# Performance work log

Measured on AMD Instinct MI355X. Metric: run time of the kernel, lower is better.

Reference implementation:

```python
import jax, jax.numpy as jnp
import numpy as np

ALPHA = 0.2          # leaky relu negative slope
NEG_BIG = -9e15      # masking value used by the torch module


def setup_inputs() -> dict:
    key = jax.random.key(0)
    k1, k2, k3, k4, k5 = jax.random.split(key, 5)
    N, F_IN, F_OUT = 8192, 256, 64
    inputs = jax.random.normal(k1, (N, F_IN), dtype=jnp.float32)
    adj = jax.random.randint(k2, (N, N), 0, 2, dtype=jnp.int32)
    # xavier-normal-ish parameter init (scale is irrelevant for correctness testing)
    W = jax.random.normal(k3, (F_IN, F_OUT), dtype=jnp.float32) * np.sqrt(2.0 / (F_IN + F_OUT))
    a1 = jax.random.normal(k4, (F_OUT, 1), dtype=jnp.float32) * np.sqrt(2.0 / (F_OUT + 1))
    a2 = jax.random.normal(k5, (F_OUT, 1), dtype=jnp.float32) * np.sqrt(2.0 / (F_OUT + 1))
    return {"inputs": inputs, "adj": adj, "W": W, "a1": a1, "a2": a2}


def reference(inputs, adj, W, a1, a2):
    # h: [N, F_OUT]
    h = inputs @ W
    f1 = h @ a1                      # [N, 1]
    f2 = h @ a2                      # [N, 1]
    e = jax.nn.leaky_relu(f1 + f2.T, negative_slope=ALPHA)   # [N, N] broadcast additive score
    e = jnp.where(adj > 0, e, NEG_BIG)
    attention = jax.nn.softmax(e, axis=-1)                    # masked softmax over rows
    # dropout is identity in eval mode (training=False)
    h_prime = attention @ h                                   # [N, F_OUT]
    return jax.nn.elu(h_prime)                                # concat=True -> elu
```

## Files before the change

kernel.cpp:

```cpp
#include <hip/hip_runtime.h>
#include <hip/hip_bf16.h>

#define N     8192
#define FIN   256
#define FOUT  64
#define ALPHA 0.2f
#define KQ    8
#define JQ    (N / KQ)
#define TJ    256
#define NTL   (JQ / TJ)
#define NSW   2

typedef __attribute__((ext_vector_type(8))) short bf16x8;
typedef __attribute__((ext_vector_type(4))) float f32x4;
typedef __attribute__((ext_vector_type(4))) int   i32x4;

static __device__ __forceinline__ unsigned short f2bf(float x) {
    union { float f; unsigned int u; } v; v.f = x;
    unsigned int r = v.u + 0x7FFFu + ((v.u >> 16) & 1u);
    return (unsigned short)(r >> 16);
}
static __device__ __forceinline__ float asf(unsigned int u) {
    union { unsigned int u; float f; } v; v.u = u; return v.f;
}
static __device__ __forceinline__ float wcalc(float f1v, float f2v, int a) {
    const float e = f1v + f2v;
    const float lr = fmaxf(e, ALPHA * e);
    const float w = __expf(lr);
    return (a > 0) ? w : 0.f;
}
static __device__ __forceinline__ void gload_lds16(const int* g, int* l) {
    __builtin_amdgcn_global_load_lds(
        (const __attribute__((address_space(1))) void*)g,
        (__attribute__((address_space(3))) void*)l,
        16, 0, 0);
}
static __device__ __forceinline__ int rowperm(int row) {
    return ((row << 1) | (row >> 3)) & 63;
}

__global__ __launch_bounds__(256) void k_h(
        const float* __restrict__ X, const float* __restrict__ W,
        const float* __restrict__ a1, const float* __restrict__ a2,
        unsigned short* __restrict__ hb,
        float* __restrict__ f1, float* __restrict__ f2) {
    const int lane = threadIdx.x & 63;
    const int wave = threadIdx.x >> 6;
    const int row0 = (blockIdx.x * 4 + wave) * 4;

    const f32x4* Xr[4];
    #pragma unroll
    for (int r = 0; r < 4; ++r)
        Xr[r] = (const f32x4*)(X + (size_t)(row0 + r) * FIN);

    float acc[4] = {0.f, 0.f, 0.f, 0.f};
    #pragma unroll 4
    for (int k4 = 0; k4 < FIN / 4; ++k4) {
        const float w0 = W[(k4 * 4 + 0) * FOUT + lane];
        const float w1 = W[(k4 * 4 + 1) * FOUT + lane];
        const float w2 = W[(k4 * 4 + 2) * FOUT + lane];
        const float w3 = W[(k4 * 4 + 3) * FOUT + lane];
        #pragma unroll
        for (int r = 0; r < 4; ++r) {
            const f32x4 xv = __builtin_nontemporal_load(&Xr[r][k4]);
            acc[r] = fmaf(xv.x, w0, acc[r]);
            acc[r] = fmaf(xv.y, w1, acc[r]);
            acc[r] = fmaf(xv.z, w2, acc[r]);
            acc[r] = fmaf(xv.w, w3, acc[r]);
        }
    }

    ushort4 hv;
    hv.x = f2bf(acc[0]); hv.y = f2bf(acc[1]);
    hv.z = f2bf(acc[2]); hv.w = f2bf(acc[3]);
    *(ushort4*)&hb[(size_t)(row0 >> 3) * 512 + lane * 8 + (row0 & 7)] = hv;

    const float a1v = a1[lane];
    const float a2v = a2[lane];
    #pragma unroll
    for (int r = 0; r < 4; ++r) {
        float p1 = acc[r] * a1v;
        float p2 = acc[r] * a2v;
        #pragma unroll
        for (int off = 32; off > 0; off >>= 1) {
            p1 += __shfl_down(p1, off);
            p2 += __shfl_down(p2, off);
        }
        if (lane == 0) { f1[row0 + r] = p1; f2[row0 + r] = p2; }
    }
}

__global__ __launch_bounds__(256) void k_attn(
        const int* __restrict__ adj, const unsigned short* __restrict__ hb,
        const float* __restrict__ f1, const float* __restrict__ f2,
        float* __restrict__ part, float* __restrict__ pden) {
    __shared__ int  tile[2][16][TJ];
    __shared__ f32x4 red[2][256];
    __shared__ float dred[4][16];

    const int t    = threadIdx.x;
    const int lane = t & 63;
    const int wv   = t >> 6;
    const int bid  = blockIdx.x;
    const int rg   = bid >> 3;
    const int q    = bid & 7;
    const int i0   = rg * 16;
    const int r    = lane & 15;
    const int kg   = lane >> 4;

    const float f1v = f1[i0 + r];
    const int jb = q * JQ;
    const int pr = rowperm(r);

    f32x4 acc[4];
    #pragma unroll
    for (int c = 0; c < 4; ++c) acc[c] = (f32x4){0.f, 0.f, 0.f, 0.f};
    float sacc = 0.f;

    #pragma unroll
    for (int rr = 0; rr < 4; ++rr) {
        const int row = wv * 4 + rr;
        gload_lds16(adj + (size_t)(i0 + row) * N + jb + (lane ^ rowperm(row)) * 4,
                    &tile[0][row][0]);
    }
    asm volatile("s_waitcnt vmcnt(0)" ::: "memory");
    __builtin_amdgcn_s_barrier();

    int buf = 0;
    for (int tt = 0; tt < NTL; ++tt) {
        const int jt = jb + tt * TJ;

        bf16x8 bfr[NSW][4];
        float4 fa[NSW], fb[NSW];
        #pragma unroll
        for (int ss = 0; ss < NSW; ++ss) {
            const int s = wv * NSW + ss;
            const float* f2s = f2 + jt + s * 32 + kg * 8;
            fa[ss] = *(const float4*)(f2s);
            fb[ss] = *(const float4*)(f2s + 4);
            const unsigned short* hs =
                hb + (size_t)((jt >> 3) + s * 4 + kg) * 512 + r * 8;
            bfr[ss][0] = *(const bf16x8*)(hs);
            bfr[ss][1] = *(const bf16x8*)(hs + 128);
            bfr[ss][2] = *(const bf16x8*)(hs + 256);
            bfr[ss][3] = *(const bf16x8*)(hs + 384);
        }
        __builtin_amdgcn_sched_barrier(0);

        if (tt + 1 < NTL) {
            #pragma unroll
            for (int rr = 0; rr < 4; ++rr) {
                const int row = wv * 4 + rr;
                gload_lds16(adj + (size_t)(i0 + row) * N + jt + TJ
                                + (lane ^ rowperm(row)) * 4,
                            &tile[buf ^ 1][row][0]);
            }
            __builtin_amdgcn_sched_barrier(0);
            asm volatile("s_waitcnt vmcnt(4)" ::: "memory");
        } else {
            asm volatile("s_waitcnt vmcnt(0)" ::: "memory");
        }
        __builtin_amdgcn_s_barrier();

        #pragma unroll
        for (int ss = 0; ss < NSW; ++ss) {
            const int s = wv * NSW + ss;
            const int g0 = s * 8 + kg * 2;
            const i32x4 a0 = *(const i32x4*)&tile[buf][r][((g0 ^ pr) & 63) * 4];
            const i32x4 a1 = *(const i32x4*)&tile[buf][r][(((g0 + 1) ^ pr) & 63) * 4];

            const float w0 = wcalc(f1v, fa[ss].x, a0.x);
            const float w1 = wcalc(f1v, fa[ss].y, a0.y);
            const float w2 = wcalc(f1v, fa[ss].z, a0.z);
            const float w3 = wcalc(f1v, fa[ss].w, a0.w);
            const float w4 = wcalc(f1v, fb[ss].x, a1.x);
            const float w5 = wcalc(f1v, fb[ss].y, a1.y);
            const float w6 = wcalc(f1v, fb[ss].z, a1.z);
            const float w7 = wcalc(f1v, fb[ss].w, a1.w);

            union { bf16x8 v; __hip_bfloat162 h2[4]; unsigned int u[4]; } af;
            af.h2[0] = __float22bfloat162_rn(make_float2(w0, w1));
            af.h2[1] = __float22bfloat162_rn(make_float2(w2, w3));
            af.h2[2] = __float22bfloat162_rn(make_float2(w4, w5));
            af.h2[3] = __float22bfloat162_rn(make_float2(w6, w7));

            float ds = 0.f;
            #pragma unroll
            for (int u = 0; u < 4; ++u)
                ds += asf(af.u[u] << 16) + asf(af.u[u] & 0xFFFF0000u);
            sacc += ds;

            acc[0] = __builtin_amdgcn_mfma_f32_16x16x32_bf16(af.v, bfr[ss][0], acc[0], 0, 0, 0);
            acc[1] = __builtin_amdgcn_mfma_f32_16x16x32_bf16(af.v, bfr[ss][1], acc[1], 0, 0, 0);
            acc[2] = __builtin_amdgcn_mfma_f32_16x16x32_bf16(af.v, bfr[ss][2], acc[2], 0, 0, 0);
            acc[3] = __builtin_amdgcn_mfma_f32_16x16x32_bf16(af.v, bfr[ss][3], acc[3], 0, 0, 0);
        }
        __builtin_amdgcn_s_barrier();
        buf ^= 1;
    }

    sacc += __shfl_xor(sacc, 16);
    sacc += __shfl_xor(sacc, 32);
    if (lane < 16) dred[wv][lane] = sacc;

    __syncthreads();
    if (wv >= 2) {
        #pragma unroll
        for (int cg = 0; cg < 4; ++cg) red[wv - 2][lane * 4 + cg] = acc[cg];
    }
    __syncthreads();
    if (wv < 2) {
        #pragma unroll
        for (int cg = 0; cg < 4; ++cg) acc[cg] += red[wv][lane * 4 + cg];
    }
    __syncthreads();
    if (wv == 1) {
        #pragma unroll
        for (int cg = 0; cg < 4; ++cg) red[0][lane * 4 + cg] = acc[cg];
    }
    __syncthreads();
    if (wv == 0) {
        #pragma unroll
        for (int cg = 0; cg < 4; ++cg) acc[cg] += red[0][lane * 4 + cg];
        #pragma unroll
        for (int cg = 0; cg < 4; ++cg)
            #pragma unroll
            for (int rr = 0; rr < 4; ++rr)
                __builtin_nontemporal_store(acc[cg][rr],
                    &part[(size_t)bid * 1024 + (kg * 4 + rr) * FOUT + cg * 16 + r]);
        if (lane < 16)
            __builtin_nontemporal_store(
                dred[0][lane] + dred[1][lane] + dred[2][lane] + dred[3][lane],
                &pden[bid * 16 + lane]);
    }
}

__global__ __launch_bounds__(256) void k_fin(
        const float* __restrict__ part, const float* __restrict__ pden,
        float* __restrict__ out) {
    const int rg = blockIdx.x;
    const int t  = threadIdx.x;
    const int r  = t >> 4;
    const int c4 = (t & 15) * 4;

    float vx = 0.f, vy = 0.f, vz = 0.f, vw = 0.f;
    float den = 0.f;
    #pragma unroll
    for (int p = 0; p < KQ; ++p) {
        const int blk = rg * KQ + p;
        const f32x4 pv = __builtin_nontemporal_load(
            (const f32x4*)&part[(size_t)blk * 1024 + r * FOUT + c4]);
        vx += pv.x; vy += pv.y; vz += pv.z; vw += pv.w;
        den += __builtin_nontemporal_load(&pden[blk * 16 + r]);
    }
    den = fmaxf(den, 1e-30f);
    const float inv = __fdividef(1.f, den);
    f32x4 o;
    const float h0 = vx * inv; o.x = (h0 > 0.f) ? h0 : (__expf(h0) - 1.f);
    const float h1 = vy * inv; o.y = (h1 > 0.f) ? h1 : (__expf(h1) - 1.f);
    const float h2 = vz * inv; o.z = (h2 > 0.f) ? h2 : (__expf(h2) - 1.f);
    const float h3 = vw * inv; o.w = (h3 > 0.f) ? h3 : (__expf(h3) - 1.f);
    __builtin_nontemporal_store(o,
        (f32x4*)&out[(size_t)(rg * 16 + r) * FOUT + c4]);
}

extern "C" void kernel_launch(void* const* d_in, const int* in_sizes, int n_in,
                              void* d_out, int out_size, void* d_ws, size_t ws_size,
                              hipStream_t stream) {
    const float* X   = (const float*)d_in[0];
    const int*   adj = (const int*)d_in[1];
    const float* W   = (const float*)d_in[2];
    const float* a1  = (const float*)d_in[3];
    const float* a2  = (const float*)d_in[4];
    float* out = (float*)d_out;

    unsigned short* hb = (unsigned short*)d_ws;
    float* f1   = (float*)((char*)d_ws + (size_t)FOUT * N * 2);
    float* f2   = f1 + N;
    float* part = f2 + N;
    float* pden = part + (size_t)(N / 16) * KQ * 1024;

    k_h   <<<N / 16, 256, 0, stream>>>(X, W, a1, a2, hb, f1, f2);
    k_attn<<<(N / 16) * KQ, 256, 0, stream>>>(adj, hb, f1, f2, part, pden);
    k_fin <<<N / 16, 256, 0, stream>>>(part, pden, out);
}
```

Before: 86.75 us.

## Process 32 rows per attention block to reuse h and f2 fragments

Each k_attn block now handles 32 destination rows instead of 16, using two accumulator sets that share the same bf16 h fragments and f2 values loaded from global memory. This halves the per-row global traffic for h/f2 and halves the grid size. The adj tile and LDS double buffer double in size, the reduction scratch now reuses the tile LDS, and launch bounds request two blocks per CU. The cost is higher register and LDS use per block and fewer blocks in flight.

Result: slower. 91.99 us (+6.0%).

```diff
diff --git a/kernel.cpp b/kernel.cpp
--- a/kernel.cpp
+++ b/kernel.cpp
@@ -10,6 +10,7 @@
 #define TJ    256
 #define NTL   (JQ / TJ)
 #define NSW   2
+#define RB    32
 
 typedef __attribute__((ext_vector_type(8))) short bf16x8;
 typedef __attribute__((ext_vector_type(4))) float f32x4;
@@ -36,7 +37,7 @@
         16, 0, 0);
 }
 static __device__ __forceinline__ int rowperm(int row) {
-    return ((row << 1) | (row >> 3)) & 63;
+    return ((row << 1) | (row >> 4)) & 63;
 }
 
 __global__ __launch_bounds__(256) void k_h(
@@ -90,13 +91,12 @@
     }
 }
 
-__global__ __launch_bounds__(256) void k_attn(
+__global__ __launch_bounds__(256, 2) void k_attn(
         const int* __restrict__ adj, const unsigned short* __restrict__ hb,
         const float* __restrict__ f1, const float* __restrict__ f2,
         float* __restrict__ part, float* __restrict__ pden) {
-    __shared__ int  tile[2][16][TJ];
-    __shared__ f32x4 red[2][256];
-    __shared__ float dred[4][16];
+    __shared__ int smem[2 * RB * TJ];
+    __shared__ float dred[4][32];
 
     const int t    = threadIdx.x;
     const int lane = t & 63;
@@ -104,24 +104,29 @@
     const int bid  = blockIdx.x;
     const int rg   = bid >> 3;
     const int q    = bid & 7;
-    const int i0   = rg * 16;
+    const int i0   = rg * RB;
     const int r    = lane & 15;
     const int kg   = lane >> 4;
 
-    const float f1v = f1[i0 + r];
+    const float f1a = f1[i0 + r];
+    const float f1b = f1[i0 + 16 + r];
     const int jb = q * JQ;
-    const int pr = rowperm(r);
-
-    f32x4 acc[4];
-    #pragma unroll
-    for (int c = 0; c < 4; ++c) acc[c] = (f32x4){0.f, 0.f, 0.f, 0.f};
-    float sacc = 0.f;
-
-    #pragma unroll
-    for (int rr = 0; rr < 4; ++rr) {
-        const int row = wv * 4 + rr;
-        gload_lds16(adj + (size_t)(i0 + row) * N + jb + (lane ^ rowperm(row)) * 4,
-                    &tile[0][row][0]);
+    const int prA = rowperm(r);
+    const int prB = rowperm(16 + r);
+
+    f32x4 accA[4], accB[4];
+    #pragma unroll
+    for (int c = 0; c < 4; ++c) {
+        accA[c] = (f32x4){0.f, 0.f, 0.f, 0.f};
+        accB[c] = (f32x4){0.f, 0.f, 0.f, 0.f};
+    }
+    float saccA = 0.f, saccB = 0.f;
+
+    #pragma unroll
+    for (int rr = 0; rr < 8; ++rr) {
+        const int row = wv * 8 + rr;
+        gload_lds16(adj + (size_t)(i0 + row) * N + jb + ((lane ^ rowperm(row)) & 63) * 4,
+                    &smem[row * TJ]);
     }
     asm volatile("s_waitcnt vmcnt(0)" ::: "memory");
     __builtin_amdgcn_s_barrier();
@@ -149,109 +154,154 @@
 
         if (tt + 1 < NTL) {
             #pragma unroll
-            for (int rr = 0; rr < 4; ++rr) {
-                const int row = wv * 4 + rr;
+            for (int rr = 0; rr < 8; ++rr) {
+                const int row = wv * 8 + rr;
                 gload_lds16(adj + (size_t)(i0 + row) * N + jt + TJ
-                                + (lane ^ rowperm(row)) * 4,
-                            &tile[buf ^ 1][row][0]);
+                                + ((lane ^ rowperm(row)) & 63) * 4,
+                            &smem[(buf ^ 1) * RB * TJ + row * TJ]);
             }
             __builtin_amdgcn_sched_barrier(0);
-            asm volatile("s_waitcnt vmcnt(4)" ::: "memory");
+            asm volatile("s_waitcnt vmcnt(8)" ::: "memory");
         } else {
             asm volatile("s_waitcnt vmcnt(0)" ::: "memory");
         }
         __builtin_amdgcn_s_barrier();
 
+        const int* tb = &smem[buf * RB * TJ];
         #pragma unroll
         for (int ss = 0; ss < NSW; ++ss) {
             const int s = wv * NSW + ss;
             const int g0 = s * 8 + kg * 2;
-            const i32x4 a0 = *(const i32x4*)&tile[buf][r][((g0 ^ pr) & 63) * 4];
-            const i32x4 a1 = *(const i32x4*)&tile[buf][r][(((g0 + 1) ^ pr) & 63) * 4];
-
-            const float w0 = wcalc(f1v, fa[ss].x, a0.x);
-            const float w1 = wcalc(f1v, fa[ss].y, a0.y);
-            const float w2 = wcalc(f1v, fa[ss].z, a0.z);
-            const float w3 = wcalc(f1v, fa[ss].w, a0.w);
-            const float w4 = wcalc(f1v, fb[ss].x, a1.x);
-            const float w5 = wcalc(f1v, fb[ss].y, a1.y);
-            const float w6 = wcalc(f1v, fb[ss].z, a1.z);
-            const float w7 = wcalc(f1v, fb[ss].w, a1.w);
-
-            union { bf16x8 v; __hip_bfloat162 h2[4]; unsigned int u[4]; } af;
-            af.h2[0] = __float22bfloat162_rn(make_float2(w0, w1));
-            af.h2[1] = __float22bfloat162_rn(make_float2(w2, w3));
-            af.h2[2] = __float22bfloat162_rn(make_float2(w4, w5));
-            af.h2[3] = __float22bfloat162_rn(make_float2(w6, w7));
-
-            float ds = 0.f;
-            #pragma unroll
-            for (int u = 0; u < 4; ++u)
-                ds += asf(af.u[u] << 16) + asf(af.u[u] & 0xFFFF0000u);
-            sacc += ds;
-
-            acc[0] = __builtin_amdgcn_mfma_f32_16x16x32_bf16(af.v, bfr[ss][0], acc[0], 0, 0, 0);
-            acc[1] = __builtin_amdgcn_mfma_f32_16x16x32_bf16(af.v, bfr[ss][1], acc[1], 0, 0, 0);
-            acc[2] = __builtin_amdgcn_mfma_f32_16x16x32_bf16(af.v, bfr[ss][2], acc[2], 0, 0, 0);
-            acc[3] = __builtin_amdgcn_mfma_f32_16x16x32_bf16(af.v, bfr[ss][3], acc[3], 0, 0, 0);
+            const i32x4 a0 = *(const i32x4*)&tb[r * TJ + ((g0 ^ prA) & 63) * 4];
+            const i32x4 a1 = *(const i32x4*)&tb[r * TJ + (((g0 + 1) ^ prA) & 63) * 4];
+            const i32x4 b0 = *(const i32x4*)&tb[(16 + r) * TJ + ((g0 ^ prB) & 63) * 4];
+            const i32x4 b1 = *(const i32x4*)&tb[(16 + r) * TJ + (((g0 + 1) ^ prB) & 63) * 4];
+
+            {
+                const float w0 = wcalc(f1a, fa[ss].x, a0.x);
+                const float w1 = wcalc(f1a, fa[ss].y, a0.y);
+                const float w2 = wcalc(f1a, fa[ss].z, a0.z);
+                const float w3 = wcalc(f1a, fa[ss].w, a0.w);
+                const float w4 = wcalc(f1a, fb[ss].x, a1.x);
+                const float w5 = wcalc(f1a, fb[ss].y, a1.y);
+                const float w6 = wcalc(f1a, fb[ss].z, a1.z);
+                const float w7 = wcalc(f1a, fb[ss].w, a1.w);
+                union { bf16x8 v; __hip_bfloat162 h2[4]; unsigned int u[4]; } af;
+                af.h2[0] = __float22bfloat162_rn(make_float2(w0, w1));
+                af.h2[1] = __float22bfloat162_rn(make_float2(w2, w3));
+                af.h2[2] = __float22bfloat162_rn(make_float2(w4, w5));
+                af.h2[3] = __float22bfloat162_rn(make_float2(w6, w7));
+                float ds = 0.f;
+                #pragma unroll
+                for (int u = 0; u < 4; ++u)
+                    ds += asf(af.u[u] << 16) + asf(af.u[u] & 0xFFFF0000u);
+                saccA += ds;
+                accA[0] = __builtin_amdgcn_mfma_f32_16x16x32_bf16(af.v, bfr[ss][0], accA[0], 0, 0, 0);
+                accA[1] = __builtin_amdgcn_mfma_f32_16x16x32_bf16(af.v, bfr[ss][1], accA[1], 0, 0, 0);
+                accA[2] = __builtin_amdgcn_mfma_f32_16x16x32_bf16(af.v, bfr[ss][2], accA[2], 0, 0, 0);
+                accA[3] = __builtin_amdgcn_mfma_f32_16x16x32_bf16(af.v, bfr[ss][3], accA[3], 0, 0, 0);
+            }
+            {
+                const float w0 = wcalc(f1b, fa[ss].x, b0.x);
+                const float w1 = wcalc(f1b, fa[ss].y, b0.y);
+                const float w2 = wcalc(f1b, fa[ss].z, b0.z);
+                const float w3 = wcalc(f1b, fa[ss].w, b0.w);
+                const float w4 = wcalc(f1b, fb[ss].x, b1.x);
+                const float w5 = wcalc(f1b, fb[ss].y, b1.y);
+                const float w6 = wcalc(f1b, fb[ss].z, b1.z);
+                const float w7 = wcalc(f1b, fb[ss].w, b1.w);
+                union { bf16x8 v; __hip_bfloat162 h2[4]; unsigned int u[4]; } af;
+                af.h2[0] = __float22bfloat162_rn(make_float2(w0, w1));
+                af.h2[1] = __float22bfloat162_rn(make_float2(w2, w3));
+                af.h2[2] = __float22bfloat162_rn(make_float2(w4, w5));
+                af.h2[3] = __float22bfloat162_rn(make_float2(w6, w7));
+                float ds = 0.f;
+                #pragma unroll
+                for (int u = 0; u < 4; ++u)
+                    ds += asf(af.u[u] << 16) + asf(af.u[u] & 0xFFFF0000u);
+                saccB += ds;
+                accB[0] = __builtin_amdgcn_mfma_f32_16x16x32_bf16(af.v, bfr[ss][0], accB[0], 0, 0, 0);
+                accB[1] = __builtin_amdgcn_mfma_f32_16x16x32_bf16(af.v, bfr[ss][1], accB[1], 0, 0, 0);
+                accB[2] = __builtin_amdgcn_mfma_f32_16x16x32_bf16(af.v, bfr[ss][2], accB[2], 0, 0, 0);
+                accB[3] = __builtin_amdgcn_mfma_f32_16x16x32_bf16(af.v, bfr[ss][3], accB[3], 0, 0, 0);
+            }
         }
         __builtin_amdgcn_s_barrier();
         buf ^= 1;
     }
 
-    sacc += __shfl_xor(sacc, 16);
-    sacc += __shfl_xor(sacc, 32);
-    if (lane < 16) dred[wv][lane] = sacc;
-
+    saccA += __shfl_xor(saccA, 16); saccA += __shfl_xor(saccA, 32);
+    saccB += __shfl_xor(saccB, 16); saccB += __shfl_xor(saccB, 32);
+    if (lane < 16) { dred[wv][lane] = saccA; dred[wv][16 + lane] = saccB; }
+
+    f32x4* redA = (f32x4*)smem;
+    f32x4* redB = (f32x4*)&smem[2048];
     __syncthreads();
     if (wv >= 2) {
         #pragma unroll
-        for (int cg = 0; cg < 4; ++cg) red[wv - 2][lane * 4 + cg] = acc[cg];
+        for (int cg = 0; cg < 4; ++cg) {
+            redA[(wv - 2) * 256 + lane * 4 + cg] = accA[cg];
+            redB[(wv - 2) * 256 + lane * 4 + cg] = accB[cg];
+        }
     }
     __syncthreads();
     if (wv < 2) {
         #pragma unroll
-        for (int cg = 0; cg < 4; ++cg) acc[cg] += red[wv][lane * 4 + cg];
+        for (int cg = 0; cg < 4; ++cg) {
+            accA[cg] += redA[wv * 256 + lane * 4 + cg];
+            accB[cg] += redB[wv * 256 + lane * 4 + cg];
+        }
     }
     __syncthreads();
     if (wv == 1) {
         #pragma unroll
-        for (int cg = 0; cg < 4; ++cg) red[0][lane * 4 + cg] = acc[cg];
+        for (int cg = 0; cg < 4; ++cg) {
+            redA[lane * 4 + cg] = accA[cg];
+            redB[lane * 4 + cg] = accB[cg];
+        }
     }
     __syncthreads();
     if (wv == 0) {
         #pragma unroll
-        for (int cg = 0; cg < 4; ++cg) acc[cg] += red[0][lane * 4 + cg];
+        for (int cg = 0; cg < 4; ++cg) {
+            accA[cg] += redA[lane * 4 + cg];
+            accB[cg] += redB[lane * 4 + cg];
+        }
         #pragma unroll
         for (int cg = 0; cg < 4; ++cg)
             #pragma unroll
-            for (int rr = 0; rr < 4; ++rr)
-                __builtin_nontemporal_store(acc[cg][rr],
-                    &part[(size_t)bid * 1024 + (kg * 4 + rr) * FOUT + cg * 16 + r]);
-        if (lane < 16)
+            for (int rr = 0; rr < 4; ++rr) {
+                __builtin_nontemporal_store(accA[cg][rr],
+                    &part[(size_t)bid * 2048 + (kg * 4 + rr) * FOUT + cg * 16 + r]);
+                __builtin_nontemporal_store(accB[cg][rr],
+                    &part[(size_t)bid * 2048 + (16 + kg * 4 + rr) * FOUT + cg * 16 + r]);
+            }
+        if (lane < 32)
             __builtin_nontemporal_store(
                 dred[0][lane] + dred[1][lane] + dred[2][lane] + dred[3][lane],
-                &pden[bid * 16 + lane]);
+                &pden[bid * 32 + lane]);
     }
 }
 
 __global__ __launch_bounds__(256) void k_fin(
         const float* __restrict__ part, const float* __restrict__ pden,
         float* __restrict__ out) {
-    const int rg = blockIdx.x;
-    const int t  = threadIdx.x;
-    const int r  = t >> 4;
-    const int c4 = (t & 15) * 4;
+    const int t   = threadIdx.x;
+    const int r   = t >> 4;
+    const int c4  = (t & 15) * 4;
+    const int i   = blockIdx.x * 16 + r;
+    const int rgb = i >> 5;
+    const int ro  = i & 31;
 
     float vx = 0.f, vy = 0.f, vz = 0.f, vw = 0.f;
     float den = 0.f;
     #pragma unroll
     for (int p = 0; p < KQ; ++p) {
-        const int blk = rg * KQ + p;
+        const int b2 = rgb * KQ + p;
         const f32x4 pv = __builtin_nontemporal_load(
-            (const f32x4*)&part[(size_t)blk * 1024 + r * FOUT + c4]);
+            (const f32x4*)&part[(size_t)b2 * 2048 + ro * FOUT + c4]);
         vx += pv.x; vy += pv.y; vz += pv.z; vw += pv.w;
-        den += __builtin_nontemporal_load(&pden[blk * 16 + r]);
+        den += __builtin_nontemporal_load(&pden[b2 * 32 + ro]);
     }
     den = fmaxf(den, 1e-30f);
     const float inv = __fdividef(1.f, den);
@@ -260,8 +310,7 @@
     const float h1 = vy * inv; o.y = (h1 > 0.f) ? h1 : (__expf(h1) - 1.f);
     const float h2 = vz * inv; o.z = (h2 > 0.f) ? h2 : (__expf(h2) - 1.f);
     const float h3 = vw * inv; o.w = (h3 > 0.f) ? h3 : (__expf(h3) - 1.f);
-    __builtin_nontemporal_store(o,
-        (f32x4*)&out[(size_t)(rg * 16 + r) * FOUT + c4]);
+    __builtin_nontemporal_store(o, (f32x4*)&out[(size_t)i * FOUT + c4]);
 }
 
 extern "C" void kernel_launch(void* const* d_in, const int* in_sizes, int n_in,
@@ -278,9 +327,9 @@
     float* f1   = (float*)((char*)d_ws + (size_t)FOUT * N * 2);
     float* f2   = f1 + N;
     float* part = f2 + N;
-    float* pden = part + (size_t)(N / 16) * KQ * 1024;
+    float* pden = part + (size_t)(N / RB) * KQ * 2048;
 
     k_h   <<<N / 16, 256, 0, stream>>>(X, W, a1, a2, hb, f1, f2);
-    k_attn<<<(N / 16) * KQ, 256, 0, stream>>>(adj, hb, f1, f2, part, pden);
+    k_attn<<<(N / RB) * KQ, 256, 0, stream>>>(adj, hb, f1, f2, part, pden);
     k_fin <<<N / 16, 256, 0, stream>>>(part, pden, out);
 }
```

## Triple-buffer adjacency tiles and register-prefetch next tile's h and f2

Applied to the files above, without the earlier changes.

Replaces the double-buffered LDS adjacency tile with a three-stage ring, so adjacency loads run two tiles ahead. The h (bf16) fragments and f2 values for the next tile are prefetched into registers while the current tile is computed. The tile loop is fully unrolled, and the reduction scratch now reuses the tile LDS. This aims to hide global-load latency behind the MFMA work, at the cost of more VGPRs and LDS per block, which launch_bounds(256,3) tries to keep in check.

After: 85.08 us (median of 2 runs). Within noise of the previous version (-1.9%).

```diff
diff --git a/kernel.cpp b/kernel.cpp
--- a/kernel.cpp
+++ b/kernel.cpp
@@ -10,6 +10,7 @@
 #define TJ    256
 #define NTL   (JQ / TJ)
 #define NSW   2
+#define TILEI (16 * TJ)
 
 typedef __attribute__((ext_vector_type(8))) short bf16x8;
 typedef __attribute__((ext_vector_type(4))) float f32x4;
@@ -90,12 +91,30 @@
     }
 }
 
-__global__ __launch_bounds__(256) void k_attn(
+static __device__ __forceinline__ void load_regs(
+        int jt, int wv, int kg, int r,
+        const float* __restrict__ f2, const unsigned short* __restrict__ hb,
+        bf16x8 (&bfr)[NSW][4], float4 (&fa)[NSW], float4 (&fb)[NSW]) {
+    #pragma unroll
+    for (int ss = 0; ss < NSW; ++ss) {
+        const int s = wv * NSW + ss;
+        const float* f2s = f2 + jt + s * 32 + kg * 8;
+        fa[ss] = *(const float4*)(f2s);
+        fb[ss] = *(const float4*)(f2s + 4);
+        const unsigned short* hs =
+            hb + (size_t)((jt >> 3) + s * 4 + kg) * 512 + r * 8;
+        bfr[ss][0] = *(const bf16x8*)(hs);
+        bfr[ss][1] = *(const bf16x8*)(hs + 128);
+        bfr[ss][2] = *(const bf16x8*)(hs + 256);
+        bfr[ss][3] = *(const bf16x8*)(hs + 384);
+    }
+}
+
+__global__ __launch_bounds__(256, 3) void k_attn(
         const int* __restrict__ adj, const unsigned short* __restrict__ hb,
         const float* __restrict__ f1, const float* __restrict__ f2,
         float* __restrict__ part, float* __restrict__ pden) {
-    __shared__ int  tile[2][16][TJ];
-    __shared__ f32x4 red[2][256];
+    __shared__ int smem[3 * TILEI];
     __shared__ float dred[4][16];
 
     const int t    = threadIdx.x;
@@ -120,63 +139,61 @@
     #pragma unroll
     for (int rr = 0; rr < 4; ++rr) {
         const int row = wv * 4 + rr;
-        gload_lds16(adj + (size_t)(i0 + row) * N + jb + (lane ^ rowperm(row)) * 4,
-                    &tile[0][row][0]);
-    }
-    asm volatile("s_waitcnt vmcnt(0)" ::: "memory");
-    __builtin_amdgcn_s_barrier();
-
-    int buf = 0;
+        gload_lds16(adj + (size_t)(i0 + row) * N + jb + ((lane ^ rowperm(row)) & 63) * 4,
+                    &smem[row * TJ]);
+    }
+    bf16x8 bcur[NSW][4], bnxt[NSW][4];
+    float4 facur[NSW], fbcur[NSW], fanxt[NSW], fbnxt[NSW];
+    load_regs(jb, wv, kg, r, f2, hb, bcur, facur, fbcur);
+    __builtin_amdgcn_sched_barrier(0);
+    #pragma unroll
+    for (int rr = 0; rr < 4; ++rr) {
+        const int row = wv * 4 + rr;
+        gload_lds16(adj + (size_t)(i0 + row) * N + jb + TJ + ((lane ^ rowperm(row)) & 63) * 4,
+                    &smem[TILEI + row * TJ]);
+    }
+    __builtin_amdgcn_sched_barrier(0);
+
+    #pragma unroll
     for (int tt = 0; tt < NTL; ++tt) {
         const int jt = jb + tt * TJ;
 
-        bf16x8 bfr[NSW][4];
-        float4 fa[NSW], fb[NSW];
-        #pragma unroll
-        for (int ss = 0; ss < NSW; ++ss) {
-            const int s = wv * NSW + ss;
-            const float* f2s = f2 + jt + s * 32 + kg * 8;
-            fa[ss] = *(const float4*)(f2s);
-            fb[ss] = *(const float4*)(f2s + 4);
-            const unsigned short* hs =
-                hb + (size_t)((jt >> 3) + s * 4 + kg) * 512 + r * 8;
-            bfr[ss][0] = *(const bf16x8*)(hs);
-            bfr[ss][1] = *(const bf16x8*)(hs + 128);
-            bfr[ss][2] = *(const bf16x8*)(hs + 256);
-            bfr[ss][3] = *(const bf16x8*)(hs + 384);
-        }
+        if (tt + 1 < NTL)
+            load_regs(jt + TJ, wv, kg, r, f2, hb, bnxt, fanxt, fbnxt);
         __builtin_amdgcn_sched_barrier(0);
 
-        if (tt + 1 < NTL) {
+        if (tt + 2 < NTL) {
             #pragma unroll
             for (int rr = 0; rr < 4; ++rr) {
                 const int row = wv * 4 + rr;
-                gload_lds16(adj + (size_t)(i0 + row) * N + jt + TJ
-                                + (lane ^ rowperm(row)) * 4,
-                            &tile[buf ^ 1][row][0]);
+                gload_lds16(adj + (size_t)(i0 + row) * N + jt + 2 * TJ
+                                + ((lane ^ rowperm(row)) & 63) * 4,
+                            &smem[((tt + 2) % 3) * TILEI + row * TJ]);
             }
             __builtin_amdgcn_sched_barrier(0);
-            asm volatile("s_waitcnt vmcnt(4)" ::: "memory");
-        } else {
-            asm volatile("s_waitcnt vmcnt(0)" ::: "memory");
-        }
+        }
+
+        if (tt + 2 < NTL)      asm volatile("s_waitcnt vmcnt(20)" ::: "memory");
+        else if (tt + 1 < NTL) asm volatile("s_waitcnt vmcnt(16)" ::: "memory");
+        else                   asm volatile("s_waitcnt vmcnt(0)"  ::: "memory");
         __builtin_amdgcn_s_barrier();
 
+        const int* tb = &smem[(tt % 3) * TILEI];
         #pragma unroll
         for (int ss = 0; ss < NSW; ++ss) {
             const int s = wv * NSW + ss;
             const int g0 = s * 8 + kg * 2;
-            const i32x4 a0 = *(const i32x4*)&tile[buf][r][((g0 ^ pr) & 63) * 4];
-            const i32x4 a1 = *(const i32x4*)&tile[buf][r][(((g0 + 1) ^ pr) & 63) * 4];
-
-            const float w0 = wcalc(f1v, fa[ss].x, a0.x);
-            const float w1 = wcalc(f1v, fa[ss].y, a0.y);
-            const float w2 = wcalc(f1v, fa[ss].z, a0.z);
-            const float w3 = wcalc(f1v, fa[ss].w, a0.w);
-            const float w4 = wcalc(f1v, fb[ss].x, a1.x);
-            const float w5 = wcalc(f1v, fb[ss].y, a1.y);
-            const float w6 = wcalc(f1v, fb[ss].z, a1.z);
-            const float w7 = wcalc(f1v, fb[ss].w, a1.w);
+            const i32x4 a0 = *(const i32x4*)&tb[r * TJ + ((g0 ^ pr) & 63) * 4];
+            const i32x4 a1 = *(const i32x4*)&tb[r * TJ + (((g0 + 1) ^ pr) & 63) * 4];
+
+            const float w0 = wcalc(f1v, facur[ss].x, a0.x);
+            const float w1 = wcalc(f1v, facur[ss].y, a0.y);
+            const float w2 = wcalc(f1v, facur[ss].z, a0.z);
+            const float w3 = wcalc(f1v, facur[ss].w, a0.w);
+            const float w4 = wcalc(f1v, fbcur[ss].x, a1.x);
+            const float w5 = wcalc(f1v, fbcur[ss].y, a1.y);
+            const float w6 = wcalc(f1v, fbcur[ss].z, a1.z);
+            const float w7 = wcalc(f1v, fbcur[ss].w, a1.w);
 
             union { bf16x8 v; __hip_bfloat162 h2[4]; unsigned int u[4]; } af;
             af.h2[0] = __float22bfloat162_rn(make_float2(w0, w1));
@@ -190,38 +207,47 @@
                 ds += asf(af.u[u] << 16) + asf(af.u[u] & 0xFFFF0000u);
             sacc += ds;
 
-            acc[0] = __builtin_amdgcn_mfma_f32_16x16x32_bf16(af.v, bfr[ss][0], acc[0], 0, 0, 0);
-            acc[1] = __builtin_amdgcn_mfma_f32_16x16x32_bf16(af.v, bfr[ss][1], acc[1], 0, 0, 0);
-            acc[2] = __builtin_amdgcn_mfma_f32_16x16x32_bf16(af.v, bfr[ss][2], acc[2], 0, 0, 0);
-            acc[3] = __builtin_amdgcn_mfma_f32_16x16x32_bf16(af.v, bfr[ss][3], acc[3], 0, 0, 0);
+            acc[0] = __builtin_amdgcn_mfma_f32_16x16x32_bf16(af.v, bcur[ss][0], acc[0], 0, 0, 0);
+            acc[1] = __builtin_amdgcn_mfma_f32_16x16x32_bf16(af.v, bcur[ss][1], acc[1], 0, 0, 0);
+            acc[2] = __builtin_amdgcn_mfma_f32_16x16x32_bf16(af.v, bcur[ss][2], acc[2], 0, 0, 0);
+            acc[3] = __builtin_amdgcn_mfma_f32_16x16x32_bf16(af.v, bcur[ss][3], acc[3], 0, 0, 0);
         }
         __builtin_amdgcn_s_barrier();
-        buf ^= 1;
+
+        if (tt + 1 < NTL) {
+            #pragma unroll
+            for (int ss = 0; ss < NSW; ++ss) {
+                bcur[ss][0] = bnxt[ss][0]; bcur[ss][1] = bnxt[ss][1];
+                bcur[ss][2] = bnxt[ss][2]; bcur[ss][3] = bnxt[ss][3];
+                facur[ss] = fanxt[ss]; fbcur[ss] = fbnxt[ss];
+            }
+        }
     }
 
     sacc += __shfl_xor(sacc, 16);
     sacc += __shfl_xor(sacc, 32);
     if (lane < 16) dred[wv][lane] = sacc;
 
+    f32x4* red = (f32x4*)smem;
     __syncthreads();
     if (wv >= 2) {
         #pragma unroll
-        for (int cg = 0; cg < 4; ++cg) red[wv - 2][lane * 4 + cg] = acc[cg];
+        for (int cg = 0; cg < 4; ++cg) red[(wv - 2) * 256 + lane * 4 + cg] = acc[cg];
     }
     __syncthreads();
     if (wv < 2) {
         #pragma unroll
-        for (int cg = 0; cg < 4; ++cg) acc[cg] += red[wv][lane * 4 + cg];
+        for (int cg = 0; cg < 4; ++cg) acc[cg] += red[wv * 256 + lane * 4 + cg];
     }
     __syncthreads();
     if (wv == 1) {
         #pragma unroll
-        for (int cg = 0; cg < 4; ++cg) red[0][lane * 4 + cg] = acc[cg];
+        for (int cg = 0; cg < 4; ++cg) red[lane * 4 + cg] = acc[cg];
     }
     __syncthreads();
     if (wv == 0) {
         #pragma unroll
-        for (int cg = 0; cg < 4; ++cg) acc[cg] += red[0][lane * 4 + cg];
+        for (int cg = 0; cg < 4; ++cg) acc[cg] += red[lane * 4 + cg];
         #pragma unroll
         for (int cg = 0; cg < 4; ++cg)
             #pragma unroll
```
